# Kernel tuning notes

Hardware: AMD Instinct MI355X
Metric: run time of the kernel (lower is better)

## Reference

```python
import jax, jax.numpy as jnp
import numpy as np

B, T, D, H, E, K = 2, 1024, 1024, 16, 8, 2
HS = D // H
FF = 4 * D


def layernorm(x, g, b, eps=1e-5):
    m = jnp.mean(x, axis=-1, keepdims=True)
    v = jnp.mean((x - m) ** 2, axis=-1, keepdims=True)
    return (x - m) * jax.lax.rsqrt(v + eps) * g + b


def setup_inputs() -> dict:
    key = jax.random.key(0)
    ks = jax.random.split(key, 10)
    s = 0.02
    return {
        "x": jax.random.normal(ks[0], (B, T, D), jnp.float32),
        "Wq": jax.random.normal(ks[1], (H, D, HS), jnp.float32) * s,
        "Wk": jax.random.normal(ks[2], (H, D, HS), jnp.float32) * s,
        "Wv": jax.random.normal(ks[3], (H, D, HS), jnp.float32) * s,
        "gate_W": jax.random.normal(ks[4], (D, E), jnp.float32) * s,
        "W1": jax.random.normal(ks[5], (E, D, FF), jnp.float32) * s,
        "b1": jnp.zeros((E, FF), jnp.float32),
        "W2": jax.random.normal(ks[6], (E, FF, D), jnp.float32) * s,
        "b2": jnp.zeros((E, D), jnp.float32),
        "ln1_g": jnp.ones((D,), jnp.float32),
        "ln1_b": jnp.zeros((D,), jnp.float32),
        "ln2_g": jnp.ones((D,), jnp.float32),
        "ln2_b": jnp.zeros((D,), jnp.float32),
    }


def reference(x, Wq, Wk, Wv, gate_W, W1, b1, W2, b2, ln1_g, ln1_b, ln2_g, ln2_b):
    b, t, d = x.shape
    # --- multi-head causal attention (note: original scales by n_embed**-0.5) ---
    q = jnp.einsum("btd,hdf->bhtf", x, Wq)
    k = jnp.einsum("btd,hdf->bhtf", x, Wk)
    v = jnp.einsum("btd,hdf->bhtf", x, Wv)
    wei = jnp.einsum("bhtf,bhsf->bhts", q, k) * (d ** -0.5)
    mask = jnp.tril(jnp.ones((t, t), bool))
    wei = jnp.where(mask, wei, -jnp.inf)
    wei = jax.nn.softmax(wei, axis=-1)
    attn = jnp.einsum("bhts,bhsf->bhtf", wei, v)
    attn = attn.transpose(0, 2, 1, 3).reshape(b, t, d)  # concat heads

    y = x + layernorm(attn, ln1_g, ln1_b)

    # --- MoE: top-k gate, softmax over selected logits, weighted combine ---
    flat = y.reshape(-1, d)                         # [N, D]
    logits = flat @ gate_W                          # [N, E]
    topv, topi = jax.lax.top_k(logits, K)           # [N, K]
    w = jax.nn.softmax(topv, axis=-1)               # [N, K]
    combine = jnp.sum(jax.nn.one_hot(topi, E, dtype=flat.dtype) * w[..., None], axis=1)  # [N, E]

    h = jax.nn.relu(jnp.einsum("nd,edf->enf", flat, W1) + b1[:, None, :])  # [E, N, FF]
    eo = jnp.einsum("enf,efd->end", h, W2) + b2[:, None, :]                # [E, N, D]
    moe = jnp.einsum("ne,end->nd", combine, eo)                            # [N, D]

    out = y + layernorm(moe.reshape(b, t, d), ln2_g, ln2_b)
    return out
```

## Files before the change

### kernel.cpp

```cpp
#include <hip/hip_runtime.h>
#include <hip/hip_bf16.h>
#include <math.h>

typedef short short8 __attribute__((ext_vector_type(8)));
typedef float floatx4 __attribute__((ext_vector_type(4)));
typedef unsigned int u32_g __attribute__((address_space(1)));
typedef unsigned int u32_l __attribute__((address_space(3)));

__device__ __forceinline__ void gl_lds16(const void* g, void* l) {
    __builtin_amdgcn_global_load_lds((const u32_g*)g, (u32_l*)l, 16, 0, 0);
}

#define NB 2
#define TSEQ 1024
#define DIM 1024
#define NHEAD 16
#define HS 64
#define NEXP 8
#define FF 4096
#define NTOK (NB*TSEQ)
#define MAXSLOT 5120

#define OFF_Q      ((size_t)0)
#define OFF_K      ((size_t)8388608)
#define OFF_V      ((size_t)16777216)
#define OFF_ATTN   ((size_t)25165824)
#define OFF_Y      ((size_t)33554432)
#define OFF_YBF    ((size_t)41943040)
#define OFF_W1T    ((size_t)46137344)
#define OFF_MOE    ((size_t)113246208)
#define OFF_TOPKE  ((size_t)121634816)
#define OFF_TOPKW  ((size_t)121651200)
#define OFF_CNT    ((size_t)121667584)
#define OFF_PO     ((size_t)121667648)
#define OFF_CUR    ((size_t)121667712)
#define OFF_SLOTT  ((size_t)121667776)
#define OFF_SLOTW  ((size_t)121688256)
#define OFF_S      ((size_t)121708800)
#define OFF_XHI    (OFF_S)
#define OFF_XLO    (OFF_S + 4194304)
#define OFF_WTHI   (OFF_S + 8388608)
#define OFF_WTLO   (OFF_S + 14680064)
#define OFF_W2T    (OFF_S)
#define OFF_H      (OFF_S + 67108864)

#define OFF_ATTNB  (OFF_Q)
#define OFF_SLOTOF (OFF_MOE)
#define OFF_EOA    (OFF_W1T)
#define OFF_EOB    (OFF_W1T + 20971520)

__global__ __launch_bounds__(256) void xsplit_kernel(
    const float* __restrict__ x, __hip_bfloat16* __restrict__ xhi, __hip_bfloat16* __restrict__ xlo)
{
    int idx = (blockIdx.x * 256 + threadIdx.x) * 4;
    float4 v = *(const float4*)(x + idx);
    float vv[4] = {v.x, v.y, v.z, v.w};
    union { ushort u[4]; ushort4 q; } hi, lo;
    #pragma unroll
    for (int l = 0; l < 4; ++l) {
        __hip_bfloat16 hb = __float2bfloat16(vv[l]);
        hi.u[l] = *(const ushort*)&hb;
        float r = vv[l] - __bfloat162float(hb);
        __hip_bfloat16 lb = __float2bfloat16(r);
        lo.u[l] = *(const ushort*)&lb;
    }
    *(ushort4*)((ushort*)xhi + idx) = hi.q;
    *(ushort4*)((ushort*)xlo + idx) = lo.q;
}

__global__ __launch_bounds__(256) void wsplit_kernel(
    const float* __restrict__ Wq, const float* __restrict__ Wk, const float* __restrict__ Wv,
    __hip_bfloat16* __restrict__ Wthi, __hip_bfloat16* __restrict__ Wtlo)
{
    int z = blockIdx.z, mat = z >> 4, hh = z & 15;
    const float* W = (mat == 0) ? Wq : ((mat == 1) ? Wk : Wv);
    const float* slab = W + (size_t)hh * DIM * HS;
    ushort* ohi = (ushort*)Wthi + (size_t)mat * (DIM * DIM) + (size_t)hh * HS * DIM;
    ushort* olo = (ushort*)Wtlo + (size_t)mat * (DIM * DIM) + (size_t)hh * HS * DIM;
    int c0 = blockIdx.x * 32, r0 = blockIdx.y * 32;
    __shared__ float tile[32][33];
    int t = threadIdx.x, i = t >> 3, j4 = (t & 7) * 4;
    float4 v4 = *(const float4*)(slab + (size_t)(r0 + i) * HS + c0 + j4);
    tile[i][j4] = v4.x; tile[i][j4+1] = v4.y; tile[i][j4+2] = v4.z; tile[i][j4+3] = v4.w;
    __syncthreads();
    union { ushort u[4]; ushort4 q; } hi, lo;
    #pragma unroll
    for (int l = 0; l < 4; ++l) {
        float xv = tile[j4 + l][i];
        __hip_bfloat16 hb = __float2bfloat16(xv);
        hi.u[l] = *(const ushort*)&hb;
        float r = xv - __bfloat162float(hb);
        __hip_bfloat16 lb = __float2bfloat16(r);
        lo.u[l] = *(const ushort*)&lb;
    }
    *(ushort4*)(ohi + (size_t)(c0 + i) * DIM + r0 + j4) = hi.q;
    *(ushort4*)(olo + (size_t)(c0 + i) * DIM + r0 + j4) = lo.q;
}

__global__ __launch_bounds__(256) void qkv_mfma(
    const __hip_bfloat16* __restrict__ xhi, const __hip_bfloat16* __restrict__ xlo,
    const __hip_bfloat16* __restrict__ Wthi, const __hip_bfloat16* __restrict__ Wtlo,
    float* __restrict__ Q, float* __restrict__ Kb, float* __restrict__ V)
{
    int mat = blockIdx.z;
    const __hip_bfloat16* Bhg = Wthi + (size_t)mat * (DIM * DIM);
    const __hip_bfloat16* Blg = Wtlo + (size_t)mat * (DIM * DIM);
    float* O = (mat == 0) ? Q : ((mat == 1) ? Kb : V);
    int n0 = blockIdx.x * 64, m0 = blockIdx.y * 128;
    int t = threadIdx.x, wave = t >> 6, lane = t & 63;
    __shared__ __hip_bfloat16 Ah[128][32];
    __shared__ __hip_bfloat16 Al[128][32];
    __shared__ __hip_bfloat16 Bh[64][32];
    __shared__ __hip_bfloat16 Bl[64][32];
    const __hip_bfloat16 *gAh[2], *gAl[2];
    __hip_bfloat16 *lAh[2], *lAl[2];
    #pragma unroll
    for (int p = 0; p < 2; ++p) {
        int lin = p * 256 + t, row = lin >> 2, seg = lin & 3;
        gAh[p] = xhi + (size_t)(m0 + row) * DIM + seg * 8;
        gAl[p] = xlo + (size_t)(m0 + row) * DIM + seg * 8;
        int cb = p * 256 + wave * 64;
        lAh[p] = &Ah[0][0] + (size_t)cb * 8;
        lAl[p] = &Al[0][0] + (size_t)cb * 8;
    }
    const __hip_bfloat16* gBh = Bhg + (size_t)(n0 + (t >> 2)) * DIM + (t & 3) * 8;
    const __hip_bfloat16* gBl = Blg + (size_t)(n0 + (t >> 2)) * DIM + (t & 3) * 8;
    __hip_bfloat16* lBh = &Bh[0][0] + (size_t)(wave * 64) * 8;
    __hip_bfloat16* lBl = &Bl[0][0] + (size_t)(wave * 64) * 8;

    int wr = (wave >> 1) * 64, wcl = (wave & 1) * 32;
    int lrow = lane & 15, quad = lane >> 4;
    floatx4 acc[4][2];
    #pragma unroll
    for (int i = 0; i < 4; ++i)
        #pragma unroll
        for (int j = 0; j < 2; ++j) acc[i][j] = (floatx4){0.f, 0.f, 0.f, 0.f};

    for (int k0 = 0; k0 < DIM; k0 += 32) {
        __syncthreads();
        gl_lds16(gAh[0] + k0, lAh[0]); gl_lds16(gAh[1] + k0, lAh[1]);
        gl_lds16(gAl[0] + k0, lAl[0]); gl_lds16(gAl[1] + k0, lAl[1]);
        gl_lds16(gBh + k0, lBh);       gl_lds16(gBl + k0, lBl);
        __syncthreads();
        short8 ah[4], al[4], bh[2], bl[2];
        #pragma unroll
        for (int i = 0; i < 4; ++i) {
            ah[i] = *(const short8*)(&Ah[wr + i * 16 + lrow][quad * 8]);
            al[i] = *(const short8*)(&Al[wr + i * 16 + lrow][quad * 8]);
        }
        #pragma unroll
        for (int j = 0; j < 2; ++j) {
            bh[j] = *(const short8*)(&Bh[wcl + j * 16 + lrow][quad * 8]);
            bl[j] = *(const short8*)(&Bl[wcl + j * 16 + lrow][quad * 8]);
        }
        #pragma unroll
        for (int i = 0; i < 4; ++i)
            #pragma unroll
            for (int j = 0; j < 2; ++j) {
                acc[i][j] = __builtin_amdgcn_mfma_f32_16x16x32_bf16(ah[i], bh[j], acc[i][j], 0, 0, 0);
                acc[i][j] = __builtin_amdgcn_mfma_f32_16x16x32_bf16(ah[i], bl[j], acc[i][j], 0, 0, 0);
                acc[i][j] = __builtin_amdgcn_mfma_f32_16x16x32_bf16(al[i], bh[j], acc[i][j], 0, 0, 0);
            }
    }
    #pragma unroll
    for (int i = 0; i < 4; ++i)
        #pragma unroll
        for (int j = 0; j < 2; ++j) {
            int ng = n0 + wcl + j * 16 + lrow;
            int hh = ng >> 6, f = ng & 63;
            #pragma unroll
            for (int r = 0; r < 4; ++r) {
                int mg = m0 + wr + i * 16 + quad * 4 + r;
                int bb = mg >> 10, tt = mg & 1023;
                O[(((size_t)bb * NHEAD + hh) * TSEQ + tt) * HS + f] = acc[i][j][r];
            }
        }
}

__global__ __launch_bounds__(256) void scores_kernel(
    const float* __restrict__ Q, const float* __restrict__ Kb, float* __restrict__ S)
{
    int tri = blockIdx.x, bh = blockIdx.y;
    int mt = 0; while (((mt + 1) * (mt + 2)) / 2 <= tri) ++mt;
    int nt = tri - (mt * (mt + 1)) / 2;
    int m0 = mt * 128, n0 = nt * 128;
    const float* Qb = Q + (size_t)bh * TSEQ * HS;
    const float* Kh = Kb + (size_t)bh * TSEQ * HS;
    float* Sb = S + (size_t)bh * TSEQ * TSEQ;
    __shared__ float As[16][132];
    __shared__ float Bs[16][132];
    int t = threadIdx.x, tx = t & 15, ty = t >> 4;
    float acc[8][8] = {{0.f}};
    for (int k0 = 0; k0 < HS; k0 += 16) {
        #pragma unroll
        for (int pss = 0; pss < 2; ++pss) {
            int lin = pss * 256 + t, m = lin >> 2, c = lin & 3;
            float4 v4 = *(const float4*)(Qb + (size_t)(m0 + m) * HS + k0 + c * 4);
            As[c*4+0][m] = v4.x; As[c*4+1][m] = v4.y; As[c*4+2][m] = v4.z; As[c*4+3][m] = v4.w;
        }
        #pragma unroll
        for (int pss = 0; pss < 2; ++pss) {
            int lin = pss * 256 + t, s = lin >> 2, c = lin & 3;
            float4 v4 = *(const float4*)(Kh + (size_t)(n0 + s) * HS + k0 + c * 4);
            Bs[c*4+0][s] = v4.x; Bs[c*4+1][s] = v4.y; Bs[c*4+2][s] = v4.z; Bs[c*4+3][s] = v4.w;
        }
        __syncthreads();
        #pragma unroll
        for (int kk = 0; kk < 16; ++kk) {
            float a[8], b[8];
            *(float4*)a       = *(const float4*)(&As[kk][ty * 4]);
            *(float4*)(a + 4) = *(const float4*)(&As[kk][64 + ty * 4]);
            *(float4*)b       = *(const float4*)(&Bs[kk][tx * 4]);
            *(float4*)(b + 4) = *(const float4*)(&Bs[kk][64 + tx * 4]);
            #pragma unroll
            for (int i = 0; i < 8; ++i)
                #pragma unroll
                for (int j = 0; j < 8; ++j) acc[i][j] += a[i] * b[j];
        }
        __syncthreads();
    }
    const float scale = 0.03125f;
    #pragma unroll
    for (int i = 0; i < 8; ++i) {
        int r = m0 + ((i < 4) ? ty * 4 + i : 64 + ty * 4 + (i - 4));
        #pragma unroll
        for (int jg = 0; jg < 2; ++jg) {
            int cb = n0 + ((jg == 0) ? tx * 4 : 64 + tx * 4);
            float4 v4 = make_float4(acc[i][jg*4+0]*scale, acc[i][jg*4+1]*scale,
                                    acc[i][jg*4+2]*scale, acc[i][jg*4+3]*scale);
            *(float4*)(Sb + (size_t)r * TSEQ + cb) = v4;
        }
    }
}

__global__ __launch_bounds__(256) void softmax_kernel(float* __restrict__ S)
{
    int row = blockIdx.x, bh = row >> 10, r = row & 1023;
    float* p = S + ((size_t)bh * TSEQ + r) * TSEQ;
    int len = r + 1, t = threadIdx.x;
    int klim = (r & ~127) + 128;
    float v[4]; float mx = -1e30f;
    #pragma unroll
    for (int i = 0; i < 4; ++i) { int c = t + i * 256; v[i] = (c < len) ? p[c] : -1e30f; mx = fmaxf(mx, v[i]); }
    __shared__ float redA[4];
    #pragma unroll
    for (int off = 32; off; off >>= 1) mx = fmaxf(mx, __shfl_down(mx, off));
    if ((t & 63) == 0) redA[t >> 6] = mx;
    __syncthreads();
    mx = fmaxf(fmaxf(redA[0], redA[1]), fmaxf(redA[2], redA[3]));
    float sum = 0.f;
    #pragma unroll
    for (int i = 0; i < 4; ++i) { int c = t + i * 256; float e = (c < len) ? expf(v[i] - mx) : 0.f; v[i] = e; sum += e; }
    __shared__ float redB[4];
    #pragma unroll
    for (int off = 32; off; off >>= 1) sum += __shfl_down(sum, off);
    if ((t & 63) == 0) redB[t >> 6] = sum;
    __syncthreads();
    float inv = 1.f / (redB[0] + redB[1] + redB[2] + redB[3]);
    #pragma unroll
    for (int i = 0; i < 4; ++i) { int c = t + i * 256; if (c < klim) p[c] = v[i] * inv; }
}

__global__ __launch_bounds__(256) void pv_kernel(
    const float* __restrict__ S, const float* __restrict__ V,
    float* __restrict__ attn, float* __restrict__ attnB)
{
    int mt = blockIdx.x, bh = blockIdx.y, z = blockIdx.z;
    int m0 = mt * 128;
    int half = (m0 >> 1) + 64;
    int kbeg = z ? half : 0;
    int kend = z ? (m0 + 128) : half;
    float* O = z ? attnB : attn;
    const float* P = S + (size_t)bh * TSEQ * TSEQ;
    const float* Vb = V + (size_t)bh * TSEQ * HS;
    __shared__ float As[16][132];
    __shared__ float Bs[16][68];
    int t = threadIdx.x, tx = t & 15, ty = t >> 4;
    float acc[8][4] = {{0.f}};
    for (int k0 = kbeg; k0 < kend; k0 += 16) {
        #pragma unroll
        for (int pss = 0; pss < 2; ++pss) {
            int lin = pss * 256 + t, m = lin >> 2, c = lin & 3;
            float4 v4 = *(const float4*)(P + (size_t)(m0 + m) * TSEQ + k0 + c * 4);
            As[c*4+0][m] = v4.x; As[c*4+1][m] = v4.y; As[c*4+2][m] = v4.z; As[c*4+3][m] = v4.w;
        }
        { int kk = t >> 4, c = t & 15;
          float4 v4 = *(const float4*)(Vb + (size_t)(k0 + kk) * HS + c * 4);
          *(float4*)(&Bs[kk][c * 4]) = v4; }
        __syncthreads();
        #pragma unroll
        for (int kk = 0; kk < 16; ++kk) {
            float a[8], b[4];
            *(float4*)a       = *(const float4*)(&As[kk][ty * 4]);
            *(float4*)(a + 4) = *(const float4*)(&As[kk][64 + ty * 4]);
            *(float4*)b       = *(const float4*)(&Bs[kk][tx * 4]);
            #pragma unroll
            for (int i = 0; i < 8; ++i)
                #pragma unroll
                for (int j = 0; j < 4; ++j) acc[i][j] += a[i] * b[j];
        }
        __syncthreads();
    }
    int b = bh >> 4, hh = bh & 15;
    #pragma unroll
    for (int i = 0; i < 8; ++i) {
        int r = m0 + ((i < 4) ? ty * 4 + i : 64 + ty * 4 + (i - 4));
        float4 v4 = make_float4(acc[i][0], acc[i][1], acc[i][2], acc[i][3]);
        *(float4*)(O + ((size_t)b * TSEQ + r) * DIM + hh * HS + tx * 4) = v4;
    }
}

__global__ __launch_bounds__(256) void ln1_kernel(
    const float* __restrict__ x, const float* __restrict__ attn, const float* __restrict__ attnB,
    const float* __restrict__ g, const float* __restrict__ bta,
    float* __restrict__ y, __hip_bfloat16* __restrict__ ybf)
{
    int n = blockIdx.x, t = threadIdx.x;
    const float* a = attn + (size_t)n * DIM;
    const float* aB = attnB + (size_t)n * DIM;
    float v[4]; float s = 0.f;
    #pragma unroll
    for (int i = 0; i < 4; ++i) { int c = t + i * 256; v[i] = a[c] + aB[c]; s += v[i]; }
    __shared__ float redA[4];
    #pragma unroll
    for (int off = 32; off; off >>= 1) s += __shfl_down(s, off);
    if ((t & 63) == 0) redA[t >> 6] = s;
    __syncthreads();
    float mean = (redA[0] + redA[1] + redA[2] + redA[3]) * (1.f / 1024.f);
    float s2 = 0.f;
    #pragma unroll
    for (int i = 0; i < 4; ++i) { float d = v[i] - mean; s2 += d * d; }
    __shared__ float redB[4];
    #pragma unroll
    for (int off = 32; off; off >>= 1) s2 += __shfl_down(s2, off);
    if ((t & 63) == 0) redB[t >> 6] = s2;
    __syncthreads();
    float rstd = rsqrtf((redB[0] + redB[1] + redB[2] + redB[3]) * (1.f / 1024.f) + 1e-5f);
    #pragma unroll
    for (int i = 0; i < 4; ++i) {
        int d = t + i * 256;
        float val = x[(size_t)n * DIM + d] + (v[i] - mean) * rstd * g[d] + bta[d];
        y[(size_t)n * DIM + d] = val;
        ybf[(size_t)n * DIM + d] = __float2bfloat16(val);
    }
}

__global__ __launch_bounds__(256) void transpose_kernel(
    const float* __restrict__ in, __hip_bfloat16* __restrict__ out, int R, int C)
{
    const float* ie = in + (size_t)blockIdx.z * R * C;
    __hip_bfloat16* oe = out + (size_t)blockIdx.z * R * C;
    int c0 = blockIdx.x * 32, r0 = blockIdx.y * 32;
    __shared__ float tile[32][33];
    int t = threadIdx.x, i = t >> 3, j4 = (t & 7) * 4;
    float4 v4 = *(const float4*)(ie + (size_t)(r0 + i) * C + c0 + j4);
    tile[i][j4] = v4.x; tile[i][j4+1] = v4.y; tile[i][j4+2] = v4.z; tile[i][j4+3] = v4.w;
    __syncthreads();
    union { ushort u[4]; ushort4 v; } pk;
    #pragma unroll
    for (int l = 0; l < 4; ++l) {
        __hip_bfloat16 hb = __float2bfloat16(tile[j4 + l][i]);
        pk.u[l] = *(const ushort*)&hb;
    }
    *(ushort4*)((ushort*)oe + (size_t)(c0 + i) * R + r0 + j4) = pk.v;
}

__global__ __launch_bounds__(256) void gate_kernel(
    const float* __restrict__ y, const float* __restrict__ gW,
    int* __restrict__ topk_e, float* __restrict__ topk_w, int* __restrict__ cnt)
{
    int n = blockIdx.x, t = threadIdx.x;
    const float* yr = y + (size_t)n * DIM;
    float p[8] = {0.f,0.f,0.f,0.f,0.f,0.f,0.f,0.f};
    for (int d = t; d < DIM; d += 256) {
        float yv = yr[d];
        const float* w = gW + (size_t)d * NEXP;
        #pragma unroll
        for (int e = 0; e < 8; ++e) p[e] += yv * w[e];
    }
    #pragma unroll
    for (int e = 0; e < 8; ++e)
        #pragma unroll
        for (int off = 32; off; off >>= 1) p[e] += __shfl_down(p[e], off);
    __shared__ float lg[4][8];
    if ((t & 63) == 0) { int w = t >> 6;
        #pragma unroll
        for (int e = 0; e < 8; ++e) lg[w][e] = p[e]; }
    __syncthreads();
    if (t == 0) {
        float l[8];
        #pragma unroll
        for (int e = 0; e < 8; ++e) l[e] = lg[0][e] + lg[1][e] + lg[2][e] + lg[3][e];
        int e0 = 0; float v0 = l[0];
        for (int e = 1; e < 8; ++e) if (l[e] > v0) { v0 = l[e]; e0 = e; }
        int e1 = 0; float v1 = -1e30f;
        for (int e = 0; e < 8; ++e) if (e != e0 && l[e] > v1) { v1 = l[e]; e1 = e; }
        float z = expf(v1 - v0);
        float w0 = 1.f / (1.f + z), w1 = z / (1.f + z);
        topk_e[n * 2] = e0; topk_e[n * 2 + 1] = e1;
        topk_w[n * 2] = w0; topk_w[n * 2 + 1] = w1;
        atomicAdd(&cnt[e0], 1); atomicAdd(&cnt[e1], 1);
    }
}

__global__ void scan_kernel(const int* __restrict__ cnt, int* __restrict__ po, int* __restrict__ cursor)
{
    if (threadIdx.x == 0 && blockIdx.x == 0) {
        int acc = 0;
        for (int e = 0; e < 8; ++e) { po[e] = acc; cursor[e] = acc; acc += ((cnt[e] + 127) >> 7) << 7; }
        po[8] = acc;
    }
}

__global__ void scatter_kernel(const int* __restrict__ topk_e, const float* __restrict__ topk_w,
                               int* __restrict__ cursor, int* __restrict__ slot_token,
                               int* __restrict__ slot_of)
{
    int i = blockIdx.x * 256 + threadIdx.x;
    int e = topk_e[i];
    int pos = atomicAdd(&cursor[e], 1);
    slot_token[pos] = i >> 1;
    slot_of[i] = pos;
}

__global__ __launch_bounds__(256) void moe_gemm1(
    const __hip_bfloat16* __restrict__ ybf, const __hip_bfloat16* __restrict__ W1t,
    const float* __restrict__ b1, const int* __restrict__ po, const int* __restrict__ cnt,
    const int* __restrict__ slot_token, __hip_bfloat16* __restrict__ h)
{
    int flat = blockIdx.x;
    int xcd = flat & 7, j = flat >> 3;
    int n0 = (((j & 3) << 3) + xcd) * 128;
    int m0 = (j >> 2) * 128;
    int total = po[8];
    if (m0 >= total) return;
    int e = 0;
    for (int i = 0; i < 8; ++i) if (m0 >= po[i] && m0 < po[i + 1]) e = i;
    int valid = po[e] + cnt[e] - m0; if (valid > 128) valid = 128;
    int t = threadIdx.x, wave = t >> 6, lane = t & 63;
    __shared__ int tok[128];
    __shared__ __hip_bfloat16 As[128][64];
    __shared__ __hip_bfloat16 Bs[128][64];
    if (t < 128) tok[t] = (t < valid) ? slot_token[m0 + t] : slot_token[m0];
    __syncthreads();
    const __hip_bfloat16 *gA[4], *gB[4];
    __hip_bfloat16 *lA[4], *lB[4];
    #pragma unroll
    for (int p = 0; p < 4; ++p) {
        int lin = p * 256 + t, row = lin >> 3, seg = lin & 7;
        gA[p] = ybf + (size_t)tok[row] * DIM + seg * 8;
        gB[p] = W1t + ((size_t)e * FF + n0 + row) * DIM + seg * 8;
        int cb = p * 256 + wave * 64;
        lA[p] = &As[0][0] + (size_t)cb * 8;
        lB[p] = &Bs[0][0] + (size_t)cb * 8;
    }
    int wr = (wave >> 1) * 64, wc = (wave & 1) * 64;
    int lrow = lane & 15, quad = lane >> 4;
    floatx4 acc[4][4];
    #pragma unroll
    for (int i = 0; i < 4; ++i)
        #pragma unroll
        for (int j2 = 0; j2 < 4; ++j2) acc[i][j2] = (floatx4){0.f, 0.f, 0.f, 0.f};
    for (int k0 = 0; k0 < DIM; k0 += 64) {
        __syncthreads();
        #pragma unroll
        for (int p = 0; p < 4; ++p) { gl_lds16(gA[p] + k0, lA[p]); gl_lds16(gB[p] + k0, lB[p]); }
        __syncthreads();
        #pragma unroll
        for (int ks = 0; ks < 2; ++ks) {
            short8 a[4], b[4];
            #pragma unroll
            for (int i = 0; i < 4; ++i) a[i] = *(const short8*)(&As[wr + i * 16 + lrow][ks * 32 + quad * 8]);
            #pragma unroll
            for (int j2 = 0; j2 < 4; ++j2) b[j2] = *(const short8*)(&Bs[wc + j2 * 16 + lrow][ks * 32 + quad * 8]);
            #pragma unroll
            for (int i = 0; i < 4; ++i)
                #pragma unroll
                for (int j2 = 0; j2 < 4; ++j2)
                    acc[i][j2] = __builtin_amdgcn_mfma_f32_16x16x32_bf16(a[i], b[j2], acc[i][j2], 0, 0, 0);
        }
    }
    #pragma unroll
    for (int i = 0; i < 4; ++i)
        #pragma unroll
        for (int j2 = 0; j2 < 4; ++j2) {
            int col = n0 + wc + j2 * 16 + lrow;
            float bias = b1[e * FF + col];
            #pragma unroll
            for (int r = 0; r < 4; ++r) {
                int row = wr + i * 16 + quad * 4 + r;
                float vv = fmaxf(acc[i][j2][r] + bias, 0.f);
                h[(size_t)(m0 + row) * FF + col] = __float2bfloat16(vv);
            }
        }
}

__global__ __launch_bounds__(256) void moe_gemm2(
    const __hip_bfloat16* __restrict__ h, const __hip_bfloat16* __restrict__ W2t,
    const float* __restrict__ b2, const int* __restrict__ po,
    float* __restrict__ eoA, float* __restrict__ eoB)
{
    int flat = blockIdx.x;
    int xcd = flat & 7, j = flat >> 3;
    int n0 = xcd * 128;
    int kz = j & 1;
    int m0 = (j >> 1) * 128;
    int total = po[8];
    if (m0 >= total) return;
    int e = 0;
    for (int i = 0; i < 8; ++i) if (m0 >= po[i] && m0 < po[i + 1]) e = i;
    int t = threadIdx.x, wave = t >> 6, lane = t & 63;
    __shared__ __hip_bfloat16 As[128][64];
    __shared__ __hip_bfloat16 Bs[128][64];
    const __hip_bfloat16 *gA[4], *gB[4];
    __hip_bfloat16 *lA[4], *lB[4];
    #pragma unroll
    for (int p = 0; p < 4; ++p) {
        int lin = p * 256 + t, row = lin >> 3, seg = lin & 7;
        gA[p] = h + (size_t)(m0 + row) * FF + seg * 8;
        gB[p] = W2t + ((size_t)e * DIM + n0 + row) * FF + seg * 8;
        int cb = p * 256 + wave * 64;
        lA[p] = &As[0][0] + (size_t)cb * 8;
        lB[p] = &Bs[0][0] + (size_t)cb * 8;
    }
    int wr = (wave >> 1) * 64, wc = (wave & 1) * 64;
    int lrow = lane & 15, quad = lane >> 4;
    floatx4 acc[4][4];
    #pragma unroll
    for (int i = 0; i < 4; ++i)
        #pragma unroll
        for (int j2 = 0; j2 < 4; ++j2) acc[i][j2] = (floatx4){0.f, 0.f, 0.f, 0.f};
    int kbeg = kz * (FF / 2), kend = kbeg + (FF / 2);
    for (int k0 = kbeg; k0 < kend; k0 += 64) {
        __syncthreads();
        #pragma unroll
        for (int p = 0; p < 4; ++p) { gl_lds16(gA[p] + k0, lA[p]); gl_lds16(gB[p] + k0, lB[p]); }
        __syncthreads();
        #pragma unroll
        for (int ks = 0; ks < 2; ++ks) {
            short8 a[4], b[4];
            #pragma unroll
            for (int i = 0; i < 4; ++i) a[i] = *(const short8*)(&As[wr + i * 16 + lrow][ks * 32 + quad * 8]);
            #pragma unroll
            for (int j2 = 0; j2 < 4; ++j2) b[j2] = *(const short8*)(&Bs[wc + j2 * 16 + lrow][ks * 32 + quad * 8]);
            #pragma unroll
            for (int i = 0; i < 4; ++i)
                #pragma unroll
                for (int j2 = 0; j2 < 4; ++j2)
                    acc[i][j2] = __builtin_amdgcn_mfma_f32_16x16x32_bf16(a[i], b[j2], acc[i][j2], 0, 0, 0);
        }
    }
    float* eo = kz ? eoB : eoA;
    #pragma unroll
    for (int i = 0; i < 4; ++i)
        #pragma unroll
        for (int j2 = 0; j2 < 4; ++j2) {
            int col = n0 + wc + j2 * 16 + lrow;
            float bias = (kz == 0) ? b2[e * DIM + col] : 0.f;
            #pragma unroll
            for (int r = 0; r < 4; ++r) {
                int row = wr + i * 16 + quad * 4 + r;
                eo[(size_t)(m0 + row) * DIM + col] = acc[i][j2][r] + bias;
            }
        }
}

__global__ __launch_bounds__(256) void ln2_kernel(
    const float* __restrict__ y,
    const float* __restrict__ eoA, const float* __restrict__ eoB,
    const int* __restrict__ slot_of, const float* __restrict__ topk_w,
    const float* __restrict__ g, const float* __restrict__ bta, float* __restrict__ out)
{
    int n = blockIdx.x, t = threadIdx.x;
    int s0 = slot_of[n * 2], s1 = slot_of[n * 2 + 1];
    float w0 = topk_w[n * 2], w1 = topk_w[n * 2 + 1];
    const float* a0 = eoA + (size_t)s0 * DIM;
    const float* b0 = eoB + (size_t)s0 * DIM;
    const float* a1 = eoA + (size_t)s1 * DIM;
    const float* b1r = eoB + (size_t)s1 * DIM;
    float v[4]; float s = 0.f;
    #pragma unroll
    for (int i = 0; i < 4; ++i) {
        int c = t + i * 256;
        v[i] = w0 * (a0[c] + b0[c]) + w1 * (a1[c] + b1r[c]);
        s += v[i];
    }
    __shared__ float redA[4];
    #pragma unroll
    for (int off = 32; off; off >>= 1) s += __shfl_down(s, off);
    if ((t & 63) == 0) redA[t >> 6] = s;
    __syncthreads();
    float mean = (redA[0] + redA[1] + redA[2] + redA[3]) * (1.f / 1024.f);
    float s2 = 0.f;
    #pragma unroll
    for (int i = 0; i < 4; ++i) { float d = v[i] - mean; s2 += d * d; }
    __shared__ float redB[4];
    #pragma unroll
    for (int off = 32; off; off >>= 1) s2 += __shfl_down(s2, off);
    if ((t & 63) == 0) redB[t >> 6] = s2;
    __syncthreads();
    float rstd = rsqrtf((redB[0] + redB[1] + redB[2] + redB[3]) * (1.f / 1024.f) + 1e-5f);
    #pragma unroll
    for (int i = 0; i < 4; ++i) {
        int d = t + i * 256;
        out[(size_t)n * DIM + d] = y[(size_t)n * DIM + d] + (v[i] - mean) * rstd * g[d] + bta[d];
    }
}

extern "C" void kernel_launch(void* const* d_in, const int* in_sizes, int n_in,
                              void* d_out, int out_size, void* d_ws, size_t ws_size,
                              hipStream_t stream)
{
    const float* x    = (const float*)d_in[0];
    const float* Wq   = (const float*)d_in[1];
    const float* Wk   = (const float*)d_in[2];
    const float* Wv   = (const float*)d_in[3];
    const float* gW   = (const float*)d_in[4];
    const float* W1   = (const float*)d_in[5];
    const float* b1   = (const float*)d_in[6];
    const float* W2   = (const float*)d_in[7];
    const float* b2   = (const float*)d_in[8];
    const float* ln1g = (const float*)d_in[9];
    const float* ln1b = (const float*)d_in[10];
    const float* ln2g = (const float*)d_in[11];
    const float* ln2b = (const float*)d_in[12];
    float* out = (float*)d_out;

    char* ws = (char*)d_ws;
    float* Q    = (float*)(ws + OFF_Q);
    float* Kb   = (float*)(ws + OFF_K);
    float* V    = (float*)(ws + OFF_V);
    float* attn = (float*)(ws + OFF_ATTN);
    float* attnB= (float*)(ws + OFF_ATTNB);
    float* y    = (float*)(ws + OFF_Y);
    __hip_bfloat16* ybf = (__hip_bfloat16*)(ws + OFF_YBF);
    __hip_bfloat16* W1t = (__hip_bfloat16*)(ws + OFF_W1T);
    int*   topk_e = (int*)(ws + OFF_TOPKE);
    float* topk_w = (float*)(ws + OFF_TOPKW);
    int*   cnt    = (int*)(ws + OFF_CNT);
    int*   po     = (int*)(ws + OFF_PO);
    int*   cur    = (int*)(ws + OFF_CUR);
    int*   slot_t = (int*)(ws + OFF_SLOTT);
    int*   slot_of= (int*)(ws + OFF_SLOTOF);
    float* S      = (float*)(ws + OFF_S);
    __hip_bfloat16* xhi  = (__hip_bfloat16*)(ws + OFF_XHI);
    __hip_bfloat16* xlo  = (__hip_bfloat16*)(ws + OFF_XLO);
    __hip_bfloat16* Wthi = (__hip_bfloat16*)(ws + OFF_WTHI);
    __hip_bfloat16* Wtlo = (__hip_bfloat16*)(ws + OFF_WTLO);
    __hip_bfloat16* W2t = (__hip_bfloat16*)(ws + OFF_W2T);
    __hip_bfloat16* h   = (__hip_bfloat16*)(ws + OFF_H);
    float* eoA = (float*)(ws + OFF_EOA);
    float* eoB = (float*)(ws + OFF_EOB);

    hipMemsetAsync(cnt, 0, 32, stream);

    xsplit_kernel<<<2048, 256, 0, stream>>>(x, xhi, xlo);
    wsplit_kernel<<<dim3(2, 32, 48), 256, 0, stream>>>(Wq, Wk, Wv, Wthi, Wtlo);
    qkv_mfma<<<dim3(16, 16, 3), 256, 0, stream>>>(xhi, xlo, Wthi, Wtlo, Q, Kb, V);
    scores_kernel<<<dim3(36, 32), 256, 0, stream>>>(Q, Kb, S);
    softmax_kernel<<<NB * NHEAD * TSEQ, 256, 0, stream>>>(S);
    pv_kernel<<<dim3(8, 32, 2), 256, 0, stream>>>(S, V, attn, attnB);
    ln1_kernel<<<NTOK, 256, 0, stream>>>(x, attn, attnB, ln1g, ln1b, y, ybf);
    gate_kernel<<<NTOK, 256, 0, stream>>>(y, gW, topk_e, topk_w, cnt);
    scan_kernel<<<1, 64, 0, stream>>>(cnt, po, cur);
    scatter_kernel<<<16, 256, 0, stream>>>(topk_e, topk_w, cur, slot_t, slot_of);
    transpose_kernel<<<dim3(128, 32, 8), 256, 0, stream>>>(W1, W1t, DIM, FF);
    moe_gemm1<<<1280, 256, 0, stream>>>(ybf, W1t, b1, po, cnt, slot_t, h);
    transpose_kernel<<<dim3(32, 128, 8), 256, 0, stream>>>(W2, W2t, FF, DIM);
    moe_gemm2<<<640, 256, 0, stream>>>(h, W2t, b2, po, eoA, eoB);
    ln2_kernel<<<NTOK, 256, 0, stream>>>(y, eoA, eoB, slot_of, topk_w, ln2g, ln2b, out);
}
```

Measured before the change: 770.7 us.

## Load MoE GEMM operands directly from global into registers, dropping LDS staging

Both MoE expert GEMM kernels stop staging A and B tiles through shared memory with global_load_lds and barriers. Each wave now loads its MFMA fragments straight from global memory with 16-byte vector loads, unrolled by two. This removes the LDS round trip and the two barriers per k-step. In exchange, operands are no longer shared between the waves of a block, so each tile row is fetched twice from global/L2, and the strided per-lane loads may coalesce less well.

```diff
diff --git a/kernel.cpp b/kernel.cpp
--- a/kernel.cpp
+++ b/kernel.cpp
@@ -438,58 +438,47 @@
     for (int i = 0; i < 8; ++i) if (m0 >= po[i] && m0 < po[i + 1]) e = i;
     int valid = po[e] + cnt[e] - m0; if (valid > 128) valid = 128;
     int t = threadIdx.x, wave = t >> 6, lane = t & 63;
-    __shared__ int tok[128];
-    __shared__ __hip_bfloat16 As[128][64];
-    __shared__ __hip_bfloat16 Bs[128][64];
-    if (t < 128) tok[t] = (t < valid) ? slot_token[m0 + t] : slot_token[m0];
-    __syncthreads();
-    const __hip_bfloat16 *gA[4], *gB[4];
-    __hip_bfloat16 *lA[4], *lB[4];
-    #pragma unroll
-    for (int p = 0; p < 4; ++p) {
-        int lin = p * 256 + t, row = lin >> 3, seg = lin & 7;
-        gA[p] = ybf + (size_t)tok[row] * DIM + seg * 8;
-        gB[p] = W1t + ((size_t)e * FF + n0 + row) * DIM + seg * 8;
-        int cb = p * 256 + wave * 64;
-        lA[p] = &As[0][0] + (size_t)cb * 8;
-        lB[p] = &Bs[0][0] + (size_t)cb * 8;
-    }
     int wr = (wave >> 1) * 64, wc = (wave & 1) * 64;
     int lrow = lane & 15, quad = lane >> 4;
+    const __hip_bfloat16* pA[4];
+    const __hip_bfloat16* pB[4];
+    #pragma unroll
+    for (int i = 0; i < 4; ++i) {
+        int r = wr + i * 16 + lrow;
+        int tk = slot_token[(r < valid) ? (m0 + r) : m0];
+        pA[i] = ybf + (size_t)tk * DIM + quad * 8;
+    }
+    #pragma unroll
+    for (int jj = 0; jj < 4; ++jj)
+        pB[jj] = W1t + ((size_t)e * FF + n0 + wc + jj * 16 + lrow) * DIM + quad * 8;
     floatx4 acc[4][4];
     #pragma unroll
     for (int i = 0; i < 4; ++i)
         #pragma unroll
-        for (int j2 = 0; j2 < 4; ++j2) acc[i][j2] = (floatx4){0.f, 0.f, 0.f, 0.f};
-    for (int k0 = 0; k0 < DIM; k0 += 64) {
-        __syncthreads();
-        #pragma unroll
-        for (int p = 0; p < 4; ++p) { gl_lds16(gA[p] + k0, lA[p]); gl_lds16(gB[p] + k0, lB[p]); }
-        __syncthreads();
-        #pragma unroll
-        for (int ks = 0; ks < 2; ++ks) {
-            short8 a[4], b[4];
-            #pragma unroll
-            for (int i = 0; i < 4; ++i) a[i] = *(const short8*)(&As[wr + i * 16 + lrow][ks * 32 + quad * 8]);
-            #pragma unroll
-            for (int j2 = 0; j2 < 4; ++j2) b[j2] = *(const short8*)(&Bs[wc + j2 * 16 + lrow][ks * 32 + quad * 8]);
-            #pragma unroll
-            for (int i = 0; i < 4; ++i)
-                #pragma unroll
-                for (int j2 = 0; j2 < 4; ++j2)
-                    acc[i][j2] = __builtin_amdgcn_mfma_f32_16x16x32_bf16(a[i], b[j2], acc[i][j2], 0, 0, 0);
-        }
+        for (int jj = 0; jj < 4; ++jj) acc[i][jj] = (floatx4){0.f, 0.f, 0.f, 0.f};
+    #pragma unroll 2
+    for (int k0 = 0; k0 < DIM; k0 += 32) {
+        short8 a[4], b[4];
+        #pragma unroll
+        for (int i = 0; i < 4; ++i) a[i] = *(const short8*)(pA[i] + k0);
+        #pragma unroll
+        for (int jj = 0; jj < 4; ++jj) b[jj] = *(const short8*)(pB[jj] + k0);
+        #pragma unroll
+        for (int i = 0; i < 4; ++i)
+            #pragma unroll
+            for (int jj = 0; jj < 4; ++jj)
+                acc[i][jj] = __builtin_amdgcn_mfma_f32_16x16x32_bf16(a[i], b[jj], acc[i][jj], 0, 0, 0);
     }
     #pragma unroll
     for (int i = 0; i < 4; ++i)
         #pragma unroll
-        for (int j2 = 0; j2 < 4; ++j2) {
-            int col = n0 + wc + j2 * 16 + lrow;
+        for (int jj = 0; jj < 4; ++jj) {
+            int col = n0 + wc + jj * 16 + lrow;
             float bias = b1[e * FF + col];
             #pragma unroll
             for (int r = 0; r < 4; ++r) {
                 int row = wr + i * 16 + quad * 4 + r;
-                float vv = fmaxf(acc[i][j2][r] + bias, 0.f);
+                float vv = fmaxf(acc[i][jj][r] + bias, 0.f);
                 h[(size_t)(m0 + row) * FF + col] = __float2bfloat16(vv);
             }
         }
@@ -510,57 +499,46 @@
     int e = 0;
     for (int i = 0; i < 8; ++i) if (m0 >= po[i] && m0 < po[i + 1]) e = i;
     int t = threadIdx.x, wave = t >> 6, lane = t & 63;
-    __shared__ __hip_bfloat16 As[128][64];
-    __shared__ __hip_bfloat16 Bs[128][64];
-    const __hip_bfloat16 *gA[4], *gB[4];
-    __hip_bfloat16 *lA[4], *lB[4];
-    #pragma unroll
-    for (int p = 0; p < 4; ++p) {
-        int lin = p * 256 + t, row = lin >> 3, seg = lin & 7;
-        gA[p] = h + (size_t)(m0 + row) * FF + seg * 8;
-        gB[p] = W2t + ((size_t)e * DIM + n0 + row) * FF + seg * 8;
-        int cb = p * 256 + wave * 64;
-        lA[p] = &As[0][0] + (size_t)cb * 8;
-        lB[p] = &Bs[0][0] + (size_t)cb * 8;
-    }
     int wr = (wave >> 1) * 64, wc = (wave & 1) * 64;
     int lrow = lane & 15, quad = lane >> 4;
+    const __hip_bfloat16* pA[4];
+    const __hip_bfloat16* pB[4];
+    #pragma unroll
+    for (int i = 0; i < 4; ++i)
+        pA[i] = h + (size_t)(m0 + wr + i * 16 + lrow) * FF + quad * 8;
+    #pragma unroll
+    for (int jj = 0; jj < 4; ++jj)
+        pB[jj] = W2t + ((size_t)e * DIM + n0 + wc + jj * 16 + lrow) * FF + quad * 8;
     floatx4 acc[4][4];
     #pragma unroll
     for (int i = 0; i < 4; ++i)
         #pragma unroll
-        for (int j2 = 0; j2 < 4; ++j2) acc[i][j2] = (floatx4){0.f, 0.f, 0.f, 0.f};
+        for (int jj = 0; jj < 4; ++jj) acc[i][jj] = (floatx4){0.f, 0.f, 0.f, 0.f};
     int kbeg = kz * (FF / 2), kend = kbeg + (FF / 2);
-    for (int k0 = kbeg; k0 < kend; k0 += 64) {
-        __syncthreads();
-        #pragma unroll
-        for (int p = 0; p < 4; ++p) { gl_lds16(gA[p] + k0, lA[p]); gl_lds16(gB[p] + k0, lB[p]); }
-        __syncthreads();
-        #pragma unroll
-        for (int ks = 0; ks < 2; ++ks) {
-            short8 a[4], b[4];
-            #pragma unroll
-            for (int i = 0; i < 4; ++i) a[i] = *(const short8*)(&As[wr + i * 16 + lrow][ks * 32 + quad * 8]);
-            #pragma unroll
-            for (int j2 = 0; j2 < 4; ++j2) b[j2] = *(const short8*)(&Bs[wc + j2 * 16 + lrow][ks * 32 + quad * 8]);
-            #pragma unroll
-            for (int i = 0; i < 4; ++i)
-                #pragma unroll
-                for (int j2 = 0; j2 < 4; ++j2)
-                    acc[i][j2] = __builtin_amdgcn_mfma_f32_16x16x32_bf16(a[i], b[j2], acc[i][j2], 0, 0, 0);
-        }
+    #pragma unroll 2
+    for (int k0 = kbeg; k0 < kend; k0 += 32) {
+        short8 a[4], b[4];
+        #pragma unroll
+        for (int i = 0; i < 4; ++i) a[i] = *(const short8*)(pA[i] + k0);
+        #pragma unroll
+        for (int jj = 0; jj < 4; ++jj) b[jj] = *(const short8*)(pB[jj] + k0);
+        #pragma unroll
+        for (int i = 0; i < 4; ++i)
+            #pragma unroll
+            for (int jj = 0; jj < 4; ++jj)
+                acc[i][jj] = __builtin_amdgcn_mfma_f32_16x16x32_bf16(a[i], b[jj], acc[i][jj], 0, 0, 0);
     }
     float* eo = kz ? eoB : eoA;
     #pragma unroll
     for (int i = 0; i < 4; ++i)
         #pragma unroll
-        for (int j2 = 0; j2 < 4; ++j2) {
-            int col = n0 + wc + j2 * 16 + lrow;
+        for (int jj = 0; jj < 4; ++jj) {
+            int col = n0 + wc + jj * 16 + lrow;
             float bias = (kz == 0) ? b2[e * DIM + col] : 0.f;
             #pragma unroll
             for (int r = 0; r < 4; ++r) {
                 int row = wr + i * 16 + quad * 4 + r;
-                eo[(size_t)(m0 + row) * DIM + col] = acc[i][j2][r] + bias;
+                eo[(size_t)(m0 + row) * DIM + col] = acc[i][jj][r] + bias;
             }
         }
 }
```

Result: slower. 927.5 us (+20.3%).
